# Performance work log

Hardware: AMD Instinct MI355X
Metric: run time of the kernel (lower is better)

The kernel has to match this reference:

```python
import jax, jax.numpy as jnp
import numpy as np

N = 8192   # num_nodes
H = 128    # hidden_dim
B = 100    # batch of events
K = 5      # num_neg_samples
TD_MAX = 10000.0
TIME_SD = jnp.array([50.0, 7.0, 15.0, 15.0])  # time_sd from forward; time_mean = 0


def setup_inputs() -> dict:
    key = jax.random.key(0)
    ks = jax.random.split(key, 16)
    p = 32.0 / N  # avg degree ~32
    A = (jax.random.uniform(ks[0], (N, N)) < p).astype(jnp.float32)
    # S init: S[v,u] = 1/D[v] for neighbors u (row-normalized A)
    S = A / (A.sum(axis=1, keepdims=True) + 1e-7)
    z0 = jax.random.normal(ks[1], (N, H)) * 0.1
    u = jax.random.randint(ks[2], (B,), 0, N)
    v = jax.random.randint(ks[3], (B,), 0, N)
    event_types = jax.random.randint(ks[4], (B,), 0, 2)
    neg_idx = jax.random.randint(ks[5], (B, 2 * K), 0, N)
    time_diff = jax.random.normal(ks[6], (B, 2, 4))
    t_bar = jax.random.uniform(ks[7], (B, N)) * 1000.0
    t = 1000.0 + 10.0 * jnp.arange(B, dtype=jnp.float32)

    def lin(k, o, i):
        k1, k2 = jax.random.split(k)
        lim = 1.0 / np.sqrt(i)
        return (jax.random.uniform(k1, (o, i), minval=-lim, maxval=lim),
                jax.random.uniform(k2, (o,), minval=-lim, maxval=lim))

    om0_w, om0_b = lin(ks[8], 1, 2 * H)
    om1_w, om1_b = lin(ks[9], 1, 2 * H)
    Wh_w, Wh_b = lin(ks[10], H, H)
    Ws_w, Ws_b = lin(ks[11], H, H)
    Wr_w, Wr_b = lin(ks[12], H, H)
    Wt_w, Wt_b = lin(ks[13], H, 4)
    return dict(u=u, v=v, event_types=event_types, neg_idx=neg_idx,
                time_diff=time_diff, t_bar=t_bar, t=t, z0=z0, A=A, S=S,
                w_t=0.5 * jnp.ones(2), alpha=0.5 * jnp.ones(2), psi=0.5 * jnp.ones(2),
                om0_w=om0_w, om0_b=om0_b, om1_w=om1_w, om1_b=om1_b,
                Wh_w=Wh_w, Wh_b=Wh_b, Ws_w=Ws_w, Ws_b=Ws_b,
                Wr_w=Wr_w, Wr_b=Wr_b, Wt_w=Wt_w, Wt_b=Wt_b)


def _forward(u, v, event_types, neg_idx, time_diff, t_bar, t, z0, A, S,
             w_t, alpha, psi, om0_w, om0_b, om1_w, om1_b,
             Wh_w, Wh_b, Ws_w, Ws_b, Wr_w, Wr_b, Wt_w, Wt_b):
    td_norm = time_diff / TIME_SD  # (td - 0) / sd

    def hawkes(zu, zv, et, td):
        # lambda = psi * log(1 + exp(g/psi)) + alpha * exp(-w_t * td/td_max)
        zc = jnp.concatenate([zu, zv], axis=-1)
        g0 = jnp.einsum('...d,d->...', zc, om0_w[0]) + om0_b[0]
        g1 = jnp.einsum('...d,d->...', zc, om1_w[0]) + om1_b[0]
        g = jnp.where(et == 0, g0, g1)
        ps, al, wt = psi[et], alpha[et], w_t[et]
        gp = jnp.clip(g / (ps + 1e-7), -75.0, 75.0)
        return ps * jnp.log1p(jnp.exp(gp)) + al * jnp.exp(-wt * (td / TD_MAX))

    ar = jnp.arange(N)

    def step(z, ev):
        u_it, v_it, et, td2, tb, t_it, neg = ev
        z_u, z_v = z[u_it], z[v_it]
        Wh_all = z @ Wh_w.T + Wh_b  # [N,H]

        def struct(node):
            # structural attention over node's neighbors (masked, not dense loop)
            mask = A[node] > 0
            q = jnp.exp(S[node]) * mask
            q = q / (q.sum() + 1e-7)
            hsig = jax.nn.sigmoid(q[:, None] * Wh_all)
            hmax = jnp.where(mask[:, None], hsig, -jnp.inf).max(axis=0)
            return jnp.where(jnp.any(mask), hmax, 0.0)

        # update of u uses struct info from v's neighborhood, and vice versa
        hs = jnp.stack([struct(v_it), struct(u_it)])  # [2,H]
        h = (hs @ Ws_w.T + Ws_b) + (jnp.stack([z_u, z_v]) @ Wr_w.T + Wr_b) + (td2 @ Wt_w.T + Wt_b)
        z_upd = jax.nn.sigmoid(h)
        z_new = z.at[u_it].set(z_upd[0]).at[v_it].set(z_upd[1])

        # negative pairs: (u, v_neg_k) then (u_neg_k, v), using z_prev
        v_neg, u_neg = neg[:K], neg[K:]
        zu_neg = jnp.concatenate([jnp.broadcast_to(z_u, (K, H)), z[u_neg]], 0)
        zv_neg = jnp.concatenate([z[v_neg], jnp.broadcast_to(z_v, (K, H))], 0)
        lt_u = jnp.concatenate([jnp.full((K,), tb[u_it]), tb[u_neg]])
        lt_v = jnp.concatenate([tb[v_neg], jnp.full((K,), tb[v_it])])
        ts_neg = t_it - jnp.maximum(lt_u, lt_v)
        ts_pos = t_it - jnp.maximum(tb[u_it], tb[v_it])

        # all-node intensity prediction (Lambda_dict path, detached in torch)
        zd = jax.lax.stop_gradient(z)
        zu_all = jnp.concatenate([jnp.broadcast_to(jax.lax.stop_gradient(z_u), (N, H)),
                                  jnp.broadcast_to(jax.lax.stop_gradient(z_v), (N, H))], 0)
        zv_all = jnp.concatenate([zd, zd], 0)
        last_t = jnp.maximum(
            jnp.concatenate([jnp.full((N,), tb[u_it]), jnp.full((N,), tb[v_it])]),
            jnp.concatenate([tb, tb]))
        lam_all = hawkes(zu_all, zv_all, jnp.full((2 * N,), et),
                         jax.lax.stop_gradient(t_it - last_t))
        m = ((ar != u_it) & (ar != v_it)).astype(lam_all.dtype)
        lam_sum = jax.lax.stop_gradient(jnp.sum(lam_all * jnp.concatenate([m, m])))

        return z_new, (z_u, z_v, zu_neg, zv_neg, ts_pos, ts_neg, lam_sum)

    _, (zu_p, zv_p, zun, zvn, ts_p, ts_n, lam_sums) = jax.lax.scan(
        step, z0, (u, v, event_types, td_norm, t_bar, t, neg_idx))

    lam_pos = hawkes(zu_p, zv_p, event_types, ts_p)            # [B]
    lam_neg = hawkes(zun, zvn, event_types[:, None], ts_n)      # [B,2K]
    return jnp.concatenate([lam_pos[:, None], lam_neg, lam_sums[:, None]], axis=1)  # [B, 2K+2]


def reference(u, v, event_types, neg_idx, time_diff, t_bar, t, z0, A, S,
              w_t, alpha, psi, om0_w, om0_b, om1_w, om1_b,
              Wh_w, Wh_b, Ws_w, Ws_b, Wr_w, Wr_b, Wt_w, Wt_b):
    return _forward(u, v, event_types, neg_idx, time_diff, t_bar, t, z0, A, S,
                    w_t, alpha, psi, om0_w, om0_b, om1_w, om1_b,
                    Wh_w, Wh_b, Ws_w, Ws_b, Wr_w, Wr_b, Wt_w, Wt_b)
```

## Files before the change

kernel.cpp:

```cpp
#include <hip/hip_runtime.h>
#include <math.h>

#define N 8192
#define H 128
#define BB 100
#define KK 5
#define MAXN 256
#define TD_MAXF 10000.0f

#define OFF_WHALLV ((size_t)N * H)
#define OFF_ZVER (OFF_WHALLV + 2 * BB * H)

__global__ __launch_bounds__(256) void prep_all_kernel(
    const float* __restrict__ Wh, const float* __restrict__ Ws,
    const float* __restrict__ Wr, const float* __restrict__ om0,
    const float* __restrict__ om1, const float* __restrict__ z0,
    float* __restrict__ WhT, float* __restrict__ WsT, float* __restrict__ WrT,
    float* __restrict__ omP, unsigned* __restrict__ flags,
    float* __restrict__ dvec0) {
  const int B0 = H * H, B1 = 2 * H * H, B2 = 3 * H * H;
  const int B3 = B2 + 2 * H, B4 = B2 + 4 * H, B5 = B4 + 4 * BB + 4;
  int idx = blockIdx.x * 256 + threadIdx.x;
  if (idx < B0) {
    int d = idx >> 7, k = idx & (H - 1);
    WhT[k * H + d] = Wh[d * H + k];
  } else if (idx < B1) {
    int e = idx - B0;
    int d = e >> 7, k = e & (H - 1);
    WsT[k * H + d] = Ws[d * H + k];
  } else if (idx < B2) {
    int e = idx - B1;
    int d = e >> 7, k = e & (H - 1);
    WrT[k * H + d] = Wr[d * H + k];
  } else if (idx < B3) {
    int e = idx - B2;
    omP[e] = om0[e];
  } else if (idx < B4) {
    int e = idx - B3;
    omP[2 * H + e] = om1[e];
  } else if (idx < B5) {
    flags[idx - B4] = 0u;
  } else if (idx < B5 + N) {
    int j = idx - B5;
    const float4* zr = (const float4*)(z0 + (size_t)j * H);
    const float4* o0 = (const float4*)om0;
    const float4* o1 = (const float4*)om1;
    float a0 = 0, b0 = 0, a1 = 0, b1 = 0;
    for (int k = 0; k < H / 4; ++k) {
      float4 zv = zr[k];
      float4 l0 = o0[k], r0 = o0[k + H / 4];
      float4 l1 = o1[k], r1 = o1[k + H / 4];
      a0 += zv.x * l0.x + zv.y * l0.y + zv.z * l0.z + zv.w * l0.w;
      b0 += zv.x * r0.x + zv.y * r0.y + zv.z * r0.z + zv.w * r0.w;
      a1 += zv.x * l1.x + zv.y * l1.y + zv.z * l1.z + zv.w * l1.w;
      b1 += zv.x * r1.x + zv.y * r1.y + zv.z * r1.z + zv.w * r1.w;
    }
    dvec0[0 * N + j] = a0;
    dvec0[1 * N + j] = b0;
    dvec0[2 * N + j] = a1;
    dvec0[3 * N + j] = b1;
  }
}

__global__ __launch_bounds__(256) void build_kernel(
    const float* __restrict__ z0, const float* __restrict__ WhT,
    const float* __restrict__ Wh_b, float* __restrict__ whall,
    const int* __restrict__ u_, const int* __restrict__ v_,
    const float* __restrict__ A, const float* __restrict__ S,
    int* __restrict__ cnt, int* __restrict__ nidx, float* __restrict__ nes,
    float* __restrict__ qsum, int* __restrict__ woff, int* __restrict__ zsrc,
    unsigned* __restrict__ need) {
  const int blk = blockIdx.x;
  const int tid = threadIdx.x;
  __shared__ float zr2[2][H];
  __shared__ int cnts[256];
  __shared__ int excl[257];
  __shared__ float ssum[256];
  __shared__ int nidxL[MAXN];
  __shared__ int uL[BB], vL[BB];

  if (blk < N / 2) {
    int r = tid >> 7, d = tid & (H - 1);
    int row = blk * 2 + r;
    zr2[r][d] = z0[(size_t)row * H + d];
    __syncthreads();
    float acc = Wh_b[d];
#pragma unroll 8
    for (int k = 0; k < H; ++k) acc += zr2[r][k] * WhT[k * H + d];
    whall[(size_t)row * H + d] = acc;
    return;
  }

  const int l = blk - N / 2;
  const int b = l >> 1, r = l & 1;
  const int node = r ? u_[b] : v_[b];
  int c = 0;
  float local = 0.0f;
  unsigned hitmask = 0u;
  for (int it = 0; it < N / 256; ++it) {
    int j = it * 256 + tid;
    if (A[(size_t)node * N + j] > 0.0f) {
      hitmask |= (1u << it);
      ++c;
      local += expf(S[(size_t)node * N + j]);
    }
  }
  cnts[tid] = c;
  ssum[tid] = local;
  __syncthreads();
  if (tid == 0) {
    int s = 0;
    for (int i = 0; i < 256; ++i) { excl[i] = s; s += cnts[i]; }
    excl[256] = s;
  }
  __syncthreads();
  int p = excl[tid];
  for (int it = 0; it < N / 256; ++it) {
    if ((hitmask >> it) & 1u) {
      int j = it * 256 + tid;
      if (p < MAXN) {
        nidx[l * MAXN + p] = j;
        nidxL[p] = j;
        nes[l * MAXN + p] = expf(S[(size_t)node * N + j]);
      }
      ++p;
    }
  }
  if (tid < BB) {
    uL[tid] = u_[tid];
    vL[tid] = v_[tid];
  }
  __syncthreads();
  for (int s = 128; s > 0; s >>= 1) {
    if (tid < s) ssum[tid] += ssum[tid + s];
    __syncthreads();
  }
  const int cM = min(excl[256], MAXN);
  if (tid == 0) {
    cnt[l] = cM;
    qsum[l] = ssum[0];
  }
  for (int i = tid; i < cM; i += 256) {
    int n = nidxL[i];
    int a = -1, row = 0;
    for (int s = b - 1; s >= 0; --s) {
      if (vL[s] == n) { a = s; row = 1; break; }
      if (uL[s] == n) { a = s; row = 0; break; }
    }
    int off;
    if (a < 0) {
      off = n * H;
    } else {
      off = (int)OFF_WHALLV + (2 * a + row) * H;
      atomicOr(&need[b * 4 + (a >> 5)], 1u << (a & 31));
    }
    woff[l * MAXN + i] = off;
  }
  if (r == 0 && tid >= 254) {
    int which = tid - 254;
    int nd = which ? vL[b] : uL[b];
    int a = -1, row = 0;
    for (int s = b - 1; s >= 0; --s) {
      if (vL[s] == nd) { a = s; row = 1; break; }
      if (uL[s] == nd) { a = s; row = 0; break; }
    }
    int sv = -1;
    if (a >= 0) {
      sv = 2 * a + row;
      atomicOr(&need[b * 4 + (a >> 5)], 1u << (a & 31));
    }
    zsrc[2 * b + which] = sv;
  }
}

__global__ __launch_bounds__(1024) void fused_kernel(
    const int* __restrict__ u_, const int* __restrict__ v_,
    const int* __restrict__ et_, const int* __restrict__ neg_,
    const float* __restrict__ time_diff, const float* __restrict__ t_bar,
    const float* __restrict__ tt, const float* __restrict__ z0,
    const float* __restrict__ WhT, const float* __restrict__ WsT,
    const float* __restrict__ WrT, const float* __restrict__ omP,
    const float* __restrict__ Wh_b, const float* __restrict__ Ws_b,
    const float* __restrict__ Wr_b, const float* __restrict__ Wt_w,
    const float* __restrict__ Wt_b, const float* __restrict__ w_t,
    const float* __restrict__ alpha, const float* __restrict__ psi,
    const float* __restrict__ om0_b, const float* __restrict__ om1_b,
    const float* __restrict__ wsf, float* __restrict__ zver,
    float* __restrict__ whallv, float* __restrict__ dlog,
    const float* __restrict__ qsum_, const int* __restrict__ cnt_,
    const float* __restrict__ nes_, const int* __restrict__ woff_,
    const int* __restrict__ zsrc_, const float* __restrict__ dvec0,
    const unsigned* __restrict__ need, unsigned* done,
    float* __restrict__ out) {
  const int blk = blockIdx.x;
  const int t = threadIdx.x;
  __shared__ float scratch[8][2][H];
  __shared__ float hsS[2][H];
  __shared__ float zrowS[2][H];
  __shared__ float zupdS[2][H];
  __shared__ float td2S[2][4];
  __shared__ int woffS[2][MAXN];
  __shared__ float nqS[2][MAXN];
  __shared__ int cntS[2];
  __shared__ int uvS[2];
  __shared__ float dR[N];
  __shared__ int uS[BB], vS[BB];
  __shared__ float red[1024];
  __shared__ float suS, svS;

  if (blk < BB) {
    const int b = blk;
    const int r = t >> 9;
    const int sub = (t >> 7) & 3;
    const int d = t & (H - 1);
    const int l = 2 * b + r;
    const int c = cnt_[l];
    const float iq = 1.0f / (qsum_[l] + 1e-7f);
    const int ks = t >> 7;
    const int k0 = ks * 16;

    if (t < 512) {
      int rr = t >> 8, i = t & 255;
      woffS[rr][i] = woff_[(2 * b + rr) * MAXN + i];
      nqS[rr][i] = nes_[(2 * b + rr) * MAXN + i];
    } else if (t < 520) {
      int i = t - 512;
      int cc = i & 3;
      float sd = (cc == 0) ? 50.0f : ((cc == 1) ? 7.0f : 15.0f);
      td2S[i >> 2][cc] = time_diff[b * 8 + i] / sd;
    } else if (t < 522) {
      cntS[t - 520] = cnt_[2 * b + (t - 520)];
    } else if (t == 522) {
      uvS[0] = u_[b];
    } else if (t == 523) {
      uvS[1] = v_[b];
    }
    float wsReg[16], wrReg[16], whReg[16];
#pragma unroll
    for (int kk = 0; kk < 16; ++kk) {
      wsReg[kk] = WsT[(k0 + kk) * H + d];
      wrReg[kk] = WrT[(k0 + kk) * H + d];
      whReg[kk] = WhT[(k0 + kk) * H + d];
    }
    float biasReg = 0.0f, whbReg = 0.0f;
    float4 wt4Reg = {0.0f, 0.0f, 0.0f, 0.0f};
    float zpre = 0.0f;
    int zs = -1;
    if (t < 256) {
      int dd = t & (H - 1);
      biasReg = Ws_b[dd] + Wr_b[dd] + Wt_b[dd];
      whbReg = Wh_b[dd];
      wt4Reg = ((const float4*)Wt_w)[dd];
      int rr = t >> 7;
      zs = zsrc_[2 * b + rr];
      if (zs < 0) {
        int nd = rr ? v_[b] : u_[b];
        zpre = z0[(size_t)nd * H + dd];
      }
    }
    float omA = 0.0f, omB = 0.0f;
    if (t >= 256 && t < 768) {
      int w = (t - 256) >> 6;
      int lane = t & 63;
      int which = w & 3;
      int wsel = which >> 1;
      int offo = (which & 1) * H;
      omA = omP[wsel * 2 * H + offo + lane];
      omB = omP[wsel * 2 * H + offo + 64 + lane];
    }
    __syncthreads();

    float mx = -INFINITY;
    for (int i = sub; i < c; i += 4) {
      int off = woffS[r][i];
      if (off < (int)OFF_WHALLV)
        mx = fmaxf(mx, nqS[r][i] * iq * wsf[(size_t)off + d]);
    }
    if (t == 0) {
      for (int w = 0; w < 4; ++w) {
        unsigned nw = need[b * 4 + w];
        if (!nw) continue;
        while ((__hip_atomic_load(&done[w], __ATOMIC_RELAXED,
                                  __HIP_MEMORY_SCOPE_AGENT) &
                nw) != nw)
          __builtin_amdgcn_s_sleep(1);
      }
      __threadfence();
    }
    __syncthreads();

    const int ub = uvS[0], vb = uvS[1];

    for (int i = sub; i < c; i += 4) {
      int off = woffS[r][i];
      if (off >= (int)OFF_WHALLV)
        mx = fmaxf(mx, nqS[r][i] * iq * wsf[(size_t)off + d]);
    }
    scratch[sub][r][d] = mx;
    if (t < 256) {
      int rr = t >> 7, dd = t & (H - 1);
      zrowS[rr][dd] = (zs < 0) ? zpre : wsf[OFF_ZVER + (size_t)zs * H + dd];
    }
    __syncthreads();

    if (t < 2 * H) {
      int rr = t >> 7, dd = t & (H - 1);
      float m = fmaxf(fmaxf(scratch[0][rr][dd], scratch[1][rr][dd]),
                      fmaxf(scratch[2][rr][dd], scratch[3][rr][dd]));
      hsS[rr][dd] = (cntS[rr] > 0) ? (1.0f / (1.0f + expf(-m))) : 0.0f;
    }
    __syncthreads();

    {
      float a0 = 0.0f, a1 = 0.0f;
#pragma unroll
      for (int kk = 0; kk < 16; ++kk) {
        int k = k0 + kk;
        a0 += hsS[0][k] * wsReg[kk] + zrowS[0][k] * wrReg[kk];
        a1 += hsS[1][k] * wsReg[kk] + zrowS[1][k] * wrReg[kk];
      }
      scratch[ks][0][d] = a0;
      scratch[ks][1][d] = a1;
    }
    __syncthreads();

    if (t < 2 * H) {
      int rr = t >> 7, dd = t & (H - 1);
      float acc = biasReg;
#pragma unroll
      for (int kx = 0; kx < 8; ++kx) acc += scratch[kx][rr][dd];
      acc += td2S[rr][0] * wt4Reg.x + td2S[rr][1] * wt4Reg.y +
             td2S[rr][2] * wt4Reg.z + td2S[rr][3] * wt4Reg.w;
      float zu = 1.0f / (1.0f + expf(-acc));
      zupdS[rr][dd] = zu;
      zver[(size_t)(2 * b + rr) * H + dd] = zu;
    }
    __syncthreads();

    {
      int r0 = (ub == vb) ? 1 : 0;
      float f0 = 0.0f, f1 = 0.0f;
#pragma unroll
      for (int kk = 0; kk < 16; ++kk) {
        int k = k0 + kk;
        f0 += zupdS[r0][k] * whReg[kk];
        f1 += zupdS[1][k] * whReg[kk];
      }
      scratch[ks][0][d] = f0;
      scratch[ks][1][d] = f1;
    }
    __syncthreads();

    if (t < 2 * H) {
      int rr = t >> 7, dd = t & (H - 1);
      float acc = whbReg;
#pragma unroll
      for (int kx = 0; kx < 8; ++kx) acc += scratch[kx][rr][dd];
      whallv[(size_t)(2 * b + rr) * H + dd] = acc;
    } else if (t < 768) {
      int w = (t - 256) >> 6;
      int lane = t & 63;
      int row = w >> 2;
      int which = w & 3;
      int rr = (row == 0 && ub == vb) ? 1 : row;
      float val = zupdS[rr][lane] * omA + zupdS[rr][64 + lane] * omB;
      for (int s = 32; s > 0; s >>= 1) val += __shfl_down(val, s);
      if (lane == 0) dlog[b * 8 + which * 2 + row] = val;
    }
    __syncthreads();

    if (t == 0) {
      __threadfence();
      atomicOr(&done[b >> 5], 1u << (b & 31));
    }
    return;
  }

  const int b = blk - BB;
  const int e = et_[b];
  const int ub = u_[b], vb = v_[b];
  const float ps = psi[e], al = alpha[e], wt = w_t[e];
  const float ob0 = om0_b[0], ob1 = om1_b[0];
  const float ob = e ? ob1 : ob0;
  const float tcur = tt[b];
  const float inv_ps = 1.0f / (ps + 1e-7f);
  const int whichR = 2 * e + 1;
  const int whichL = 2 * e;

  if (t < BB) {
    uS[t] = u_[t];
    vS[t] = v_[t];
  }
  {
    const float4* base = (const float4*)(dvec0 + (size_t)whichR * N);
    float4* dst = (float4*)dR;
    for (int i = t; i < N / 4; i += 1024) dst[i] = base[i];
  }
  if (t == 0) {
    for (int w = 0; w < 4; ++w) {
      int cb = b - 32 * w;
      unsigned nw =
          (cb >= 32) ? 0xffffffffu : (cb <= 0 ? 0u : ((1u << cb) - 1u));
      if (!nw) continue;
      while ((__hip_atomic_load(&done[w], __ATOMIC_RELAXED,
                                __HIP_MEMORY_SCOPE_AGENT) &
              nw) != nw)
        __builtin_amdgcn_s_sleep(1);
    }
    __threadfence();
  }
  __syncthreads();

  for (int i = t; i < b; i += 1024) {
    int ui = uS[i], vi = vS[i];
    bool u_over = (ui == vi);
    bool v_over = false;
    for (int j = i + 1; j < b; ++j) {
      int uj = uS[j], vj = vS[j];
      u_over = u_over || (uj == ui) || (vj == ui);
      v_over = v_over || (uj == vi) || (vj == vi);
    }
    if (!u_over) dR[ui] = dlog[i * 8 + whichR * 2 + 0];
    if (!v_over) dR[vi] = dlog[i * 8 + whichR * 2 + 1];
  }

  if (t < 13) {
    auto dpre = [&](int x, int which) -> float {
      for (int bp = b - 1; bp >= 0; --bp) {
        if (vS[bp] == x) return dlog[bp * 8 + which * 2 + 1];
        if (uS[bp] == x) return dlog[bp * 8 + which * 2 + 0];
      }
      return dvec0[(size_t)which * N + x];
    };
    if (t < 11) {
      int li, ri;
      float ltu, ltv;
      if (t == 0) {
        li = ub; ri = vb;
        ltu = t_bar[(size_t)b * N + ub];
        ltv = t_bar[(size_t)b * N + vb];
      } else if (t <= 5) {
        int vn = neg_[b * (2 * KK) + (t - 1)];
        li = ub; ri = vn;
        ltu = t_bar[(size_t)b * N + ub];
        ltv = t_bar[(size_t)b * N + vn];
      } else {
        int un = neg_[b * (2 * KK) + (t - 1)];
        li = un; ri = vb;
        ltu = t_bar[(size_t)b * N + un];
        ltv = t_bar[(size_t)b * N + vb];
      }
      float g = dpre(li, whichL) + dpre(ri, whichR) + ob;
      float gp = fminf(fmaxf(g * inv_ps, -75.0f), 75.0f);
      float ts = tcur - fmaxf(ltu, ltv);
      out[b * 12 + t] = ps * log1pf(expf(gp)) + al * expf(-wt * (ts / TD_MAXF));
    } else if (t == 11) {
      suS = dpre(ub, whichL);
    } else {
      svS = dpre(vb, whichL);
    }
  }
  __syncthreads();

  const float su = suS, sv = svS;
  const float tb_u = t_bar[(size_t)b * N + ub];
  const float tb_v = t_bar[(size_t)b * N + vb];
  const float Ku = expf((su + ob) * inv_ps);
  const float Kv = expf((sv + ob) * inv_ps);
  const float Cx = al * expf(-wt * (tcur / TD_MAXF));
  const float Eu = expf(wt * (tb_u / TD_MAXF));
  const float Ev = expf(wt * (tb_v / TD_MAXF));
  const float wTD = wt / TD_MAXF;
  const float4* tb4 = (const float4*)(t_bar + (size_t)b * N);
  const float4* dR4 = (const float4*)dR;
  float acc = 0.0f;
  for (int j4 = t; j4 < N / 4; j4 += 1024) {
    float4 dv = dR4[j4];
    float4 tb = tb4[j4];
    float de[4] = {dv.x, dv.y, dv.z, dv.w};
    float te[4] = {tb.x, tb.y, tb.z, tb.w};
#pragma unroll
    for (int ee = 0; ee < 4; ++ee) {
      int j = j4 * 4 + ee;
      if (j == ub || j == vb) continue;
      float Dj = expf(de[ee] * inv_ps);
      float spl = ps * (log1pf(Ku * Dj) + log1pf(Kv * Dj));
      float Ej = expf(wTD * te[ee]);
      float ex = Cx * (fmaxf(Eu, Ej) + fmaxf(Ev, Ej));
      acc += spl + ex;
    }
  }
  red[t] = acc;
  __syncthreads();
  for (int s = 512; s > 0; s >>= 1) {
    if (t < s) red[t] += red[t + s];
    __syncthreads();
  }
  if (t == 0) out[b * 12 + 11] = red[0];
}

extern "C" void kernel_launch(void* const* d_in, const int* in_sizes, int n_in,
                              void* d_out, int out_size, void* d_ws,
                              size_t ws_size, hipStream_t stream) {
  const int* u = (const int*)d_in[0];
  const int* v = (const int*)d_in[1];
  const int* et = (const int*)d_in[2];
  const int* neg = (const int*)d_in[3];
  const float* time_diff = (const float*)d_in[4];
  const float* t_bar = (const float*)d_in[5];
  const float* t = (const float*)d_in[6];
  const float* z0 = (const float*)d_in[7];
  const float* A = (const float*)d_in[8];
  const float* S = (const float*)d_in[9];
  const float* w_t = (const float*)d_in[10];
  const float* alpha = (const float*)d_in[11];
  const float* psi = (const float*)d_in[12];
  const float* om0_w = (const float*)d_in[13];
  const float* om0_b = (const float*)d_in[14];
  const float* om1_w = (const float*)d_in[15];
  const float* om1_b = (const float*)d_in[16];
  const float* Wh_w = (const float*)d_in[17];
  const float* Wh_b = (const float*)d_in[18];
  const float* Ws_w = (const float*)d_in[19];
  const float* Ws_b = (const float*)d_in[20];
  const float* Wr_w = (const float*)d_in[21];
  const float* Wr_b = (const float*)d_in[22];
  const float* Wt_w = (const float*)d_in[23];
  const float* Wt_b = (const float*)d_in[24];
  float* out = (float*)d_out;

  float* wsf = (float*)d_ws;
  float* whall = wsf;
  float* whallv = wsf + OFF_WHALLV;
  float* zver = wsf + OFF_ZVER;
  float* WhT = zver + 2 * BB * H;
  float* WsT = WhT + H * H;
  float* WrT = WsT + H * H;
  float* omP = WrT + H * H;
  float* dvec0 = omP + 4 * H;
  float* dlog = dvec0 + 4 * N;
  float* qsum = dlog + 8 * BB;
  int* cnt = (int*)(qsum + 2 * BB);
  int* nidx = cnt + 2 * BB;
  float* nes = (float*)(nidx + 2 * BB * MAXN);
  int* woff = (int*)(nes + 2 * BB * MAXN);
  int* zsrc = woff + 2 * BB * MAXN;
  unsigned* need = (unsigned*)(zsrc + 2 * BB);
  unsigned* done = need + 4 * BB;

  const int PREP_ELEMS = 3 * H * H + 4 * H + 4 * BB + 4 + N;
  prep_all_kernel<<<(PREP_ELEMS + 255) / 256, 256, 0, stream>>>(
      Wh_w, Ws_w, Wr_w, om0_w, om1_w, z0, WhT, WsT, WrT, omP, need, dvec0);
  build_kernel<<<N / 2 + 2 * BB, 256, 0, stream>>>(
      z0, WhT, Wh_b, whall, u, v, A, S, cnt, nidx, nes, qsum, woff, zsrc,
      need);
  fused_kernel<<<2 * BB, 1024, 0, stream>>>(
      u, v, et, neg, time_diff, t_bar, t, z0, WhT, WsT, WrT, omP, Wh_b, Ws_b,
      Wr_b, Wt_w, Wt_b, w_t, alpha, psi, om0_b, om1_b, wsf, zver, whallv,
      dlog, qsum, cnt, nes, woff, zsrc, dvec0, need, done, out);
}
```

Baseline: 603.3 us.

## Fold neighbor build and on-demand Wh projection into fused kernel, drop prep kernels

Removes the build kernel that precomputed Wh·z for all 8192 nodes and the separate neighbor-list construction, along with the weight transposes. The fused kernel now scans its own adjacency rows, builds the neighbor lists with wave-level prefix sums, and computes Wh·z only for the sampled neighbors, using a padded shared-memory copy of Wh. This avoids a full N×H×H matmul and a large workspace round trip. In exchange, each event block does more serial work, such as redundant Wh projections for neighbors shared across events, and uses much more shared memory, which may limit occupancy.

```diff
diff --git a/kernel.cpp b/kernel.cpp
--- a/kernel.cpp
+++ b/kernel.cpp
@@ -10,167 +10,34 @@
 
 #define OFF_WHALLV ((size_t)N * H)
 #define OFF_ZVER (OFF_WHALLV + 2 * BB * H)
-
-__global__ __launch_bounds__(256) void prep_all_kernel(
-    const float* __restrict__ Wh, const float* __restrict__ Ws,
-    const float* __restrict__ Wr, const float* __restrict__ om0,
-    const float* __restrict__ om1, const float* __restrict__ z0,
-    float* __restrict__ WhT, float* __restrict__ WsT, float* __restrict__ WrT,
-    float* __restrict__ omP, unsigned* __restrict__ flags,
-    float* __restrict__ dvec0) {
-  const int B0 = H * H, B1 = 2 * H * H, B2 = 3 * H * H;
-  const int B3 = B2 + 2 * H, B4 = B2 + 4 * H, B5 = B4 + 4 * BB + 4;
-  int idx = blockIdx.x * 256 + threadIdx.x;
-  if (idx < B0) {
-    int d = idx >> 7, k = idx & (H - 1);
-    WhT[k * H + d] = Wh[d * H + k];
-  } else if (idx < B1) {
-    int e = idx - B0;
-    int d = e >> 7, k = e & (H - 1);
-    WsT[k * H + d] = Ws[d * H + k];
-  } else if (idx < B2) {
-    int e = idx - B1;
-    int d = e >> 7, k = e & (H - 1);
-    WrT[k * H + d] = Wr[d * H + k];
-  } else if (idx < B3) {
-    int e = idx - B2;
-    omP[e] = om0[e];
-  } else if (idx < B4) {
-    int e = idx - B3;
-    omP[2 * H + e] = om1[e];
-  } else if (idx < B5) {
-    flags[idx - B4] = 0u;
-  } else if (idx < B5 + N) {
-    int j = idx - B5;
-    const float4* zr = (const float4*)(z0 + (size_t)j * H);
-    const float4* o0 = (const float4*)om0;
-    const float4* o1 = (const float4*)om1;
-    float a0 = 0, b0 = 0, a1 = 0, b1 = 0;
-    for (int k = 0; k < H / 4; ++k) {
-      float4 zv = zr[k];
-      float4 l0 = o0[k], r0 = o0[k + H / 4];
-      float4 l1 = o1[k], r1 = o1[k + H / 4];
-      a0 += zv.x * l0.x + zv.y * l0.y + zv.z * l0.z + zv.w * l0.w;
-      b0 += zv.x * r0.x + zv.y * r0.y + zv.z * r0.z + zv.w * r0.w;
-      a1 += zv.x * l1.x + zv.y * l1.y + zv.z * l1.z + zv.w * l1.w;
-      b1 += zv.x * r1.x + zv.y * r1.y + zv.z * r1.z + zv.w * r1.w;
-    }
-    dvec0[0 * N + j] = a0;
-    dvec0[1 * N + j] = b0;
-    dvec0[2 * N + j] = a1;
-    dvec0[3 * N + j] = b1;
-  }
-}
-
-__global__ __launch_bounds__(256) void build_kernel(
-    const float* __restrict__ z0, const float* __restrict__ WhT,
-    const float* __restrict__ Wh_b, float* __restrict__ whall,
-    const int* __restrict__ u_, const int* __restrict__ v_,
-    const float* __restrict__ A, const float* __restrict__ S,
-    int* __restrict__ cnt, int* __restrict__ nidx, float* __restrict__ nes,
-    float* __restrict__ qsum, int* __restrict__ woff, int* __restrict__ zsrc,
-    unsigned* __restrict__ need) {
-  const int blk = blockIdx.x;
-  const int tid = threadIdx.x;
-  __shared__ float zr2[2][H];
-  __shared__ int cnts[256];
-  __shared__ int excl[257];
-  __shared__ float ssum[256];
-  __shared__ int nidxL[MAXN];
-  __shared__ int uL[BB], vL[BB];
-
-  if (blk < N / 2) {
-    int r = tid >> 7, d = tid & (H - 1);
-    int row = blk * 2 + r;
-    zr2[r][d] = z0[(size_t)row * H + d];
-    __syncthreads();
-    float acc = Wh_b[d];
-#pragma unroll 8
-    for (int k = 0; k < H; ++k) acc += zr2[r][k] * WhT[k * H + d];
-    whall[(size_t)row * H + d] = acc;
+#define WH_LDW 132
+
+__global__ __launch_bounds__(256) void prep2_kernel(
+    const float* __restrict__ z0, const float* __restrict__ om0,
+    const float* __restrict__ om1, float* __restrict__ dvec0,
+    unsigned* __restrict__ done) {
+  if (blockIdx.x == 32) {
+    if (threadIdx.x < 4) done[threadIdx.x] = 0u;
     return;
   }
-
-  const int l = blk - N / 2;
-  const int b = l >> 1, r = l & 1;
-  const int node = r ? u_[b] : v_[b];
-  int c = 0;
-  float local = 0.0f;
-  unsigned hitmask = 0u;
-  for (int it = 0; it < N / 256; ++it) {
-    int j = it * 256 + tid;
-    if (A[(size_t)node * N + j] > 0.0f) {
-      hitmask |= (1u << it);
-      ++c;
-      local += expf(S[(size_t)node * N + j]);
-    }
-  }
-  cnts[tid] = c;
-  ssum[tid] = local;
-  __syncthreads();
-  if (tid == 0) {
-    int s = 0;
-    for (int i = 0; i < 256; ++i) { excl[i] = s; s += cnts[i]; }
-    excl[256] = s;
-  }
-  __syncthreads();
-  int p = excl[tid];
-  for (int it = 0; it < N / 256; ++it) {
-    if ((hitmask >> it) & 1u) {
-      int j = it * 256 + tid;
-      if (p < MAXN) {
-        nidx[l * MAXN + p] = j;
-        nidxL[p] = j;
-        nes[l * MAXN + p] = expf(S[(size_t)node * N + j]);
-      }
-      ++p;
-    }
-  }
-  if (tid < BB) {
-    uL[tid] = u_[tid];
-    vL[tid] = v_[tid];
-  }
-  __syncthreads();
-  for (int s = 128; s > 0; s >>= 1) {
-    if (tid < s) ssum[tid] += ssum[tid + s];
-    __syncthreads();
-  }
-  const int cM = min(excl[256], MAXN);
-  if (tid == 0) {
-    cnt[l] = cM;
-    qsum[l] = ssum[0];
-  }
-  for (int i = tid; i < cM; i += 256) {
-    int n = nidxL[i];
-    int a = -1, row = 0;
-    for (int s = b - 1; s >= 0; --s) {
-      if (vL[s] == n) { a = s; row = 1; break; }
-      if (uL[s] == n) { a = s; row = 0; break; }
-    }
-    int off;
-    if (a < 0) {
-      off = n * H;
-    } else {
-      off = (int)OFF_WHALLV + (2 * a + row) * H;
-      atomicOr(&need[b * 4 + (a >> 5)], 1u << (a & 31));
-    }
-    woff[l * MAXN + i] = off;
-  }
-  if (r == 0 && tid >= 254) {
-    int which = tid - 254;
-    int nd = which ? vL[b] : uL[b];
-    int a = -1, row = 0;
-    for (int s = b - 1; s >= 0; --s) {
-      if (vL[s] == nd) { a = s; row = 1; break; }
-      if (uL[s] == nd) { a = s; row = 0; break; }
-    }
-    int sv = -1;
-    if (a >= 0) {
-      sv = 2 * a + row;
-      atomicOr(&need[b * 4 + (a >> 5)], 1u << (a & 31));
-    }
-    zsrc[2 * b + which] = sv;
-  }
+  int j = blockIdx.x * 256 + threadIdx.x;
+  const float4* zr = (const float4*)(z0 + (size_t)j * H);
+  const float4* o0 = (const float4*)om0;
+  const float4* o1 = (const float4*)om1;
+  float a0 = 0, b0 = 0, a1 = 0, b1 = 0;
+  for (int k = 0; k < H / 4; ++k) {
+    float4 zv = zr[k];
+    float4 l0 = o0[k], r0 = o0[k + H / 4];
+    float4 l1 = o1[k], r1 = o1[k + H / 4];
+    a0 += zv.x * l0.x + zv.y * l0.y + zv.z * l0.z + zv.w * l0.w;
+    b0 += zv.x * r0.x + zv.y * r0.y + zv.z * r0.z + zv.w * r0.w;
+    a1 += zv.x * l1.x + zv.y * l1.y + zv.z * l1.z + zv.w * l1.w;
+    b1 += zv.x * r1.x + zv.y * r1.y + zv.z * r1.z + zv.w * r1.w;
+  }
+  dvec0[0 * N + j] = a0;
+  dvec0[1 * N + j] = b0;
+  dvec0[2 * N + j] = a1;
+  dvec0[3 * N + j] = b1;
 }
 
 __global__ __launch_bounds__(1024) void fused_kernel(
@@ -178,107 +45,202 @@
     const int* __restrict__ et_, const int* __restrict__ neg_,
     const float* __restrict__ time_diff, const float* __restrict__ t_bar,
     const float* __restrict__ tt, const float* __restrict__ z0,
-    const float* __restrict__ WhT, const float* __restrict__ WsT,
-    const float* __restrict__ WrT, const float* __restrict__ omP,
-    const float* __restrict__ Wh_b, const float* __restrict__ Ws_b,
-    const float* __restrict__ Wr_b, const float* __restrict__ Wt_w,
-    const float* __restrict__ Wt_b, const float* __restrict__ w_t,
-    const float* __restrict__ alpha, const float* __restrict__ psi,
-    const float* __restrict__ om0_b, const float* __restrict__ om1_b,
-    const float* __restrict__ wsf, float* __restrict__ zver,
-    float* __restrict__ whallv, float* __restrict__ dlog,
-    const float* __restrict__ qsum_, const int* __restrict__ cnt_,
-    const float* __restrict__ nes_, const int* __restrict__ woff_,
-    const int* __restrict__ zsrc_, const float* __restrict__ dvec0,
-    const unsigned* __restrict__ need, unsigned* done,
-    float* __restrict__ out) {
+    const float* __restrict__ A, const float* __restrict__ S,
+    const float* __restrict__ Wh, const float* __restrict__ Ws,
+    const float* __restrict__ Wr, const float* __restrict__ Wh_b,
+    const float* __restrict__ Ws_b, const float* __restrict__ Wr_b,
+    const float* __restrict__ Wt_w, const float* __restrict__ Wt_b,
+    const float* __restrict__ w_t, const float* __restrict__ alpha,
+    const float* __restrict__ psi, const float* __restrict__ om0_w,
+    const float* __restrict__ om1_w, const float* __restrict__ om0_b,
+    const float* __restrict__ om1_b, const float* __restrict__ wsf,
+    float* __restrict__ zver, float* __restrict__ whallv,
+    float* __restrict__ dlog, const float* __restrict__ dvec0,
+    unsigned* done, float* __restrict__ out) {
   const int blk = blockIdx.x;
   const int t = threadIdx.x;
+  __shared__ __align__(16) float WhL[H * WH_LDW];
   __shared__ float scratch[8][2][H];
   __shared__ float hsS[2][H];
   __shared__ float zrowS[2][H];
   __shared__ float zupdS[2][H];
   __shared__ float td2S[2][4];
+  __shared__ int nidxS[2][MAXN];
+  __shared__ float nqS[2][MAXN];
   __shared__ int woffS[2][MAXN];
-  __shared__ float nqS[2][MAXN];
-  __shared__ int cntS[2];
-  __shared__ int uvS[2];
+  __shared__ int cMS[2];
+  __shared__ int zsrcS[2];
+  __shared__ unsigned needS[4];
+  __shared__ int uL[BB], vL[BB];
+  __shared__ int wsumI[16];
+  __shared__ float wsumF[16];
   __shared__ float dR[N];
-  __shared__ int uS[BB], vS[BB];
   __shared__ float red[1024];
   __shared__ float suS, svS;
 
   if (blk < BB) {
     const int b = blk;
     const int r = t >> 9;
+    const int tr = t & 511;
     const int sub = (t >> 7) & 3;
     const int d = t & (H - 1);
-    const int l = 2 * b + r;
-    const int c = cnt_[l];
-    const float iq = 1.0f / (qsum_[l] + 1e-7f);
     const int ks = t >> 7;
     const int k0 = ks * 16;
 
-    if (t < 512) {
-      int rr = t >> 8, i = t & 255;
-      woffS[rr][i] = woff_[(2 * b + rr) * MAXN + i];
-      nqS[rr][i] = nes_[(2 * b + rr) * MAXN + i];
-    } else if (t < 520) {
+    if (t < BB) {
+      uL[t] = u_[t];
+      vL[t] = v_[t];
+    }
+    if (t >= 512 && t < 520) {
       int i = t - 512;
       int cc = i & 3;
       float sd = (cc == 0) ? 50.0f : ((cc == 1) ? 7.0f : 15.0f);
       td2S[i >> 2][cc] = time_diff[b * 8 + i] / sd;
-    } else if (t < 522) {
-      cntS[t - 520] = cnt_[2 * b + (t - 520)];
-    } else if (t == 522) {
-      uvS[0] = u_[b];
-    } else if (t == 523) {
-      uvS[1] = v_[b];
-    }
+    }
+    if (t >= 1020) needS[t - 1020] = 0u;
+    {
+      const float4* wh4 = (const float4*)Wh;
+      float4* whl4 = (float4*)WhL;
+      for (int i = t; i < H * H / 4; i += 1024)
+        whl4[(i >> 5) * 33 + (i & 31)] = wh4[i];
+    }
+    const float whb = Wh_b[d];
     float wsReg[16], wrReg[16], whReg[16];
 #pragma unroll
     for (int kk = 0; kk < 16; ++kk) {
-      wsReg[kk] = WsT[(k0 + kk) * H + d];
-      wrReg[kk] = WrT[(k0 + kk) * H + d];
-      whReg[kk] = WhT[(k0 + kk) * H + d];
-    }
-    float biasReg = 0.0f, whbReg = 0.0f;
+      wsReg[kk] = Ws[(size_t)d * H + k0 + kk];
+      wrReg[kk] = Wr[(size_t)d * H + k0 + kk];
+      whReg[kk] = Wh[(size_t)d * H + k0 + kk];
+    }
+    float biasReg = 0.0f;
     float4 wt4Reg = {0.0f, 0.0f, 0.0f, 0.0f};
+    if (t < 256) {
+      int dd = t & (H - 1);
+      biasReg = Ws_b[dd] + Wr_b[dd] + Wt_b[dd];
+      wt4Reg = ((const float4*)Wt_w)[dd];
+    }
+    float omA = 0.0f, omB = 0.0f;
+    if (t >= 256 && t < 768) {
+      int w = (t - 256) >> 6;
+      int lane6 = t & 63;
+      int which = w & 3;
+      int wsel = which >> 1;
+      int offo = (which & 1) * H;
+      const float* omw = wsel ? om1_w : om0_w;
+      omA = omw[offo + lane6];
+      omB = omw[offo + 64 + lane6];
+    }
+
+    const int node = r ? u_[b] : v_[b];
+    unsigned hm = 0u;
+    int c = 0;
+    float local = 0.0f;
+    for (int it = 0; it < N / 512; ++it) {
+      int j = it * 512 + tr;
+      if (A[(size_t)node * N + j] > 0.0f) {
+        hm |= 1u << it;
+        ++c;
+        local += expf(S[(size_t)node * N + j]);
+      }
+    }
+    const int lane = t & 63;
+    const int wv = t >> 6;
+    int ex = c;
+    for (int s2 = 1; s2 < 64; s2 <<= 1) {
+      int o = __shfl_up(ex, s2);
+      if (lane >= s2) ex += o;
+    }
+    float ls = local;
+    for (int s2 = 32; s2 > 0; s2 >>= 1) ls += __shfl_down(ls, s2);
+    if (lane == 63) wsumI[wv] = ex;
+    if (lane == 0) wsumF[wv] = ls;
+    ex -= c;
+    __syncthreads();
+
+    int base0 = 0, ctot = 0;
+    float qs = 0.0f;
+    {
+      int w0 = r * 8;
+#pragma unroll
+      for (int w = 0; w < 8; ++w) {
+        int wi = w0 + w;
+        int cw = wsumI[wi];
+        if (wi < wv) base0 += cw;
+        ctot += cw;
+        qs += wsumF[wi];
+      }
+    }
+    const float iq = 1.0f / (qs + 1e-7f);
+    int p = base0 + ex;
+    for (int it = 0; it < N / 512; ++it) {
+      if ((hm >> it) & 1u) {
+        int j = it * 512 + tr;
+        if (p < MAXN) {
+          nidxS[r][p] = j;
+          nqS[r][p] = expf(S[(size_t)node * N + j]);
+        }
+        ++p;
+      }
+    }
+    const int cM = min(ctot, MAXN);
+    if (tr == 0) cMS[r] = cM;
+    __syncthreads();
+
+    for (int i = tr; i < cM; i += 512) {
+      int n = nidxS[r][i];
+      int a = -1, row = 0;
+      for (int s2 = b - 1; s2 >= 0; --s2) {
+        if (vL[s2] == n) { a = s2; row = 1; break; }
+        if (uL[s2] == n) { a = s2; row = 0; break; }
+      }
+      woffS[r][i] = (a < 0) ? n * H : (int)OFF_WHALLV + (2 * a + row) * H;
+      nqS[r][i] *= iq;
+      if (a >= 0) atomicOr(&needS[a >> 5], 1u << (a & 31));
+    }
+    if (t < 2) {
+      int nd = t ? vL[b] : uL[b];
+      int a = -1, row = 0;
+      for (int s2 = b - 1; s2 >= 0; --s2) {
+        if (vL[s2] == nd) { a = s2; row = 1; break; }
+        if (uL[s2] == nd) { a = s2; row = 0; break; }
+      }
+      zsrcS[t] = (a >= 0) ? 2 * a + row : -1;
+      if (a >= 0) atomicOr(&needS[a >> 5], 1u << (a & 31));
+    }
+    __syncthreads();
+
     float zpre = 0.0f;
     int zs = -1;
     if (t < 256) {
-      int dd = t & (H - 1);
-      biasReg = Ws_b[dd] + Wr_b[dd] + Wt_b[dd];
-      whbReg = Wh_b[dd];
-      wt4Reg = ((const float4*)Wt_w)[dd];
-      int rr = t >> 7;
-      zs = zsrc_[2 * b + rr];
+      int rr = t >> 7, dd = t & (H - 1);
+      zs = zsrcS[rr];
       if (zs < 0) {
-        int nd = rr ? v_[b] : u_[b];
+        int nd = rr ? vL[b] : uL[b];
         zpre = z0[(size_t)nd * H + dd];
       }
     }
-    float omA = 0.0f, omB = 0.0f;
-    if (t >= 256 && t < 768) {
-      int w = (t - 256) >> 6;
-      int lane = t & 63;
-      int which = w & 3;
-      int wsel = which >> 1;
-      int offo = (which & 1) * H;
-      omA = omP[wsel * 2 * H + offo + lane];
-      omB = omP[wsel * 2 * H + offo + 64 + lane];
-    }
-    __syncthreads();
 
     float mx = -INFINITY;
-    for (int i = sub; i < c; i += 4) {
-      int off = woffS[r][i];
-      if (off < (int)OFF_WHALLV)
-        mx = fmaxf(mx, nqS[r][i] * iq * wsf[(size_t)off + d]);
+    {
+      const float4* WhL4 = (const float4*)WhL;
+      for (int i = sub; i < cM; i += 4) {
+        int off = woffS[r][i];
+        if (off < (int)OFF_WHALLV) {
+          const float4* zr4 = (const float4*)(z0 + (size_t)(off >> 7) * H);
+          float acc = whb;
+#pragma unroll 8
+          for (int m = 0; m < 32; ++m) {
+            float4 zv = zr4[m];
+            float4 wvv = WhL4[d * 33 + m];
+            acc += zv.x * wvv.x + zv.y * wvv.y + zv.z * wvv.z + zv.w * wvv.w;
+          }
+          mx = fmaxf(mx, nqS[r][i] * acc);
+        }
+      }
     }
     if (t == 0) {
       for (int w = 0; w < 4; ++w) {
-        unsigned nw = need[b * 4 + w];
+        unsigned nw = needS[w];
         if (!nw) continue;
         while ((__hip_atomic_load(&done[w], __ATOMIC_RELAXED,
                                   __HIP_MEMORY_SCOPE_AGENT) &
@@ -289,12 +251,12 @@
     }
     __syncthreads();
 
-    const int ub = uvS[0], vb = uvS[1];
-
-    for (int i = sub; i < c; i += 4) {
+    const int ub = uL[b], vb = vL[b];
+
+    for (int i = sub; i < cM; i += 4) {
       int off = woffS[r][i];
       if (off >= (int)OFF_WHALLV)
-        mx = fmaxf(mx, nqS[r][i] * iq * wsf[(size_t)off + d]);
+        mx = fmaxf(mx, nqS[r][i] * wsf[(size_t)off + d]);
     }
     scratch[sub][r][d] = mx;
     if (t < 256) {
@@ -307,7 +269,7 @@
       int rr = t >> 7, dd = t & (H - 1);
       float m = fmaxf(fmaxf(scratch[0][rr][dd], scratch[1][rr][dd]),
                       fmaxf(scratch[2][rr][dd], scratch[3][rr][dd]));
-      hsS[rr][dd] = (cntS[rr] > 0) ? (1.0f / (1.0f + expf(-m))) : 0.0f;
+      hsS[rr][dd] = (cMS[rr] > 0) ? (1.0f / (1.0f + expf(-m))) : 0.0f;
     }
     __syncthreads();
 
@@ -353,19 +315,19 @@
 
     if (t < 2 * H) {
       int rr = t >> 7, dd = t & (H - 1);
-      float acc = whbReg;
+      float acc = whb;
 #pragma unroll
       for (int kx = 0; kx < 8; ++kx) acc += scratch[kx][rr][dd];
       whallv[(size_t)(2 * b + rr) * H + dd] = acc;
     } else if (t < 768) {
       int w = (t - 256) >> 6;
-      int lane = t & 63;
+      int lane6 = t & 63;
       int row = w >> 2;
       int which = w & 3;
       int rr = (row == 0 && ub == vb) ? 1 : row;
-      float val = zupdS[rr][lane] * omA + zupdS[rr][64 + lane] * omB;
-      for (int s = 32; s > 0; s >>= 1) val += __shfl_down(val, s);
-      if (lane == 0) dlog[b * 8 + which * 2 + row] = val;
+      float val = zupdS[rr][lane6] * omA + zupdS[rr][64 + lane6] * omB;
+      for (int s2 = 32; s2 > 0; s2 >>= 1) val += __shfl_down(val, s2);
+      if (lane6 == 0) dlog[b * 8 + which * 2 + row] = val;
     }
     __syncthreads();
 
@@ -388,8 +350,8 @@
   const int whichL = 2 * e;
 
   if (t < BB) {
-    uS[t] = u_[t];
-    vS[t] = v_[t];
+    uL[t] = u_[t];
+    vL[t] = v_[t];
   }
   {
     const float4* base = (const float4*)(dvec0 + (size_t)whichR * N);
@@ -412,11 +374,11 @@
   __syncthreads();
 
   for (int i = t; i < b; i += 1024) {
-    int ui = uS[i], vi = vS[i];
+    int ui = uL[i], vi = vL[i];
     bool u_over = (ui == vi);
     bool v_over = false;
     for (int j = i + 1; j < b; ++j) {
-      int uj = uS[j], vj = vS[j];
+      int uj = uL[j], vj = vL[j];
       u_over = u_over || (uj == ui) || (vj == ui);
       v_over = v_over || (uj == vi) || (vj == vi);
     }
@@ -427,8 +389,8 @@
   if (t < 13) {
     auto dpre = [&](int x, int which) -> float {
       for (int bp = b - 1; bp >= 0; --bp) {
-        if (vS[bp] == x) return dlog[bp * 8 + which * 2 + 1];
-        if (uS[bp] == x) return dlog[bp * 8 + which * 2 + 0];
+        if (vL[bp] == x) return dlog[bp * 8 + which * 2 + 1];
+        if (uL[bp] == x) return dlog[bp * 8 + which * 2 + 0];
       }
       return dvec0[(size_t)which * N + x];
     };
@@ -486,14 +448,14 @@
       float Dj = expf(de[ee] * inv_ps);
       float spl = ps * (log1pf(Ku * Dj) + log1pf(Kv * Dj));
       float Ej = expf(wTD * te[ee]);
-      float ex = Cx * (fmaxf(Eu, Ej) + fmaxf(Ev, Ej));
-      acc += spl + ex;
+      float ex2 = Cx * (fmaxf(Eu, Ej) + fmaxf(Ev, Ej));
+      acc += spl + ex2;
     }
   }
   red[t] = acc;
   __syncthreads();
-  for (int s = 512; s > 0; s >>= 1) {
-    if (t < s) red[t] += red[t + s];
+  for (int s2 = 512; s2 > 0; s2 >>= 1) {
+    if (t < s2) red[t] += red[t + s2];
     __syncthreads();
   }
   if (t == 0) out[b * 12 + 11] = red[0];
@@ -530,32 +492,15 @@
   float* out = (float*)d_out;
 
   float* wsf = (float*)d_ws;
-  float* whall = wsf;
   float* whallv = wsf + OFF_WHALLV;
   float* zver = wsf + OFF_ZVER;
-  float* WhT = zver + 2 * BB * H;
-  float* WsT = WhT + H * H;
-  float* WrT = WsT + H * H;
-  float* omP = WrT + H * H;
-  float* dvec0 = omP + 4 * H;
+  float* dvec0 = zver + 2 * BB * H;
   float* dlog = dvec0 + 4 * N;
-  float* qsum = dlog + 8 * BB;
-  int* cnt = (int*)(qsum + 2 * BB);
-  int* nidx = cnt + 2 * BB;
-  float* nes = (float*)(nidx + 2 * BB * MAXN);
-  int* woff = (int*)(nes + 2 * BB * MAXN);
-  int* zsrc = woff + 2 * BB * MAXN;
-  unsigned* need = (unsigned*)(zsrc + 2 * BB);
-  unsigned* done = need + 4 * BB;
-
-  const int PREP_ELEMS = 3 * H * H + 4 * H + 4 * BB + 4 + N;
-  prep_all_kernel<<<(PREP_ELEMS + 255) / 256, 256, 0, stream>>>(
-      Wh_w, Ws_w, Wr_w, om0_w, om1_w, z0, WhT, WsT, WrT, omP, need, dvec0);
-  build_kernel<<<N / 2 + 2 * BB, 256, 0, stream>>>(
-      z0, WhT, Wh_b, whall, u, v, A, S, cnt, nidx, nes, qsum, woff, zsrc,
-      need);
+  unsigned* done = (unsigned*)(dlog + 8 * BB);
+
+  prep2_kernel<<<33, 256, 0, stream>>>(z0, om0_w, om1_w, dvec0, done);
   fused_kernel<<<2 * BB, 1024, 0, stream>>>(
-      u, v, et, neg, time_diff, t_bar, t, z0, WhT, WsT, WrT, omP, Wh_b, Ws_b,
-      Wr_b, Wt_w, Wt_b, w_t, alpha, psi, om0_b, om1_b, wsf, zver, whallv,
-      dlog, qsum, cnt, nes, woff, zsrc, dvec0, need, done, out);
+      u, v, et, neg, time_diff, t_bar, t, z0, A, S, Wh_w, Ws_w, Wr_w, Wh_b,
+      Ws_b, Wr_b, Wt_w, Wt_b, w_t, alpha, psi, om0_w, om1_w, om0_b, om1_b,
+      wsf, zver, whallv, dlog, dvec0, done, out);
 }
```

After: 608.3 us. About the same (+0.8%).
